# Optimization experiments

Measured on AMD Instinct MI355X. Metric: run time of the kernel, lower is better.

The kernel has to match this reference:

```python
import jax, jax.numpy as jnp
import numpy as np

IN_CHANNELS = 64
N_NODES = 100000
N_POOLED = 50000
N_EDGES = 1250000


def setup_inputs() -> dict:
    key = jax.random.key(0)
    k1, k2, k3 = jax.random.split(key, 3)
    x_abstract = jax.random.normal(k1, (N_POOLED, IN_CHANNELS), dtype=jnp.float32)
    # pooling indices: unique subset of [0, N)
    perm = jax.random.permutation(k2, N_NODES)[:N_POOLED].astype(jnp.int32)
    edge_index = jax.random.randint(k3, (2, N_EDGES), 0, N_NODES, dtype=jnp.int32)
    return {
        "x_abstract": x_abstract,
        "perm": perm,
        "edge_index": edge_index,
        "original_num_nodes": N_NODES,
    }


def reference(x_abstract, perm, edge_index, original_num_nodes):
    N = original_num_nodes
    C = x_abstract.shape[1]
    # scatter pooled features back to original node slots
    x0 = jnp.zeros((N, C), dtype=x_abstract.dtype).at[perm].set(x_abstract)
    is_missing = jnp.ones((N,), dtype=bool).at[perm].set(False)

    # undirected view: every edge contributes both directions
    tgt = jnp.concatenate([edge_index[0], edge_index[1]])  # [2E]
    src = jnp.concatenate([edge_index[1], edge_index[0]])  # [2E]

    # deduplicate (tgt, src) pairs (torch.unique on neighbor ids) via lexsort + adjacent-diff mask
    order = jnp.lexsort((src, tgt))
    t_s = tgt[order]
    s_s = src[order]
    uniq = jnp.concatenate(
        [jnp.array([True]), (t_s[1:] != t_s[:-1]) | (s_s[1:] != s_s[:-1])]
    )
    # drop self loops (neighbor_ids != idx), weight 1 for each unique neighbor pair
    w = (uniq & (t_s != s_s)).astype(x_abstract.dtype)  # [2E]

    # scatter-mean of unique-neighbor features per target node
    feat_sum = jax.ops.segment_sum(x0[s_s] * w[:, None], t_s, num_segments=N)  # [N, C]
    cnt = jax.ops.segment_sum(w, t_s, num_segments=N)  # [N]
    mean = feat_sum / jnp.maximum(cnt, 1.0)[:, None]

    # only missing nodes with at least one neighbor get filled; others keep their value
    fill = is_missing & (cnt > 0)
    return jnp.where(fill[:, None], mean, x0)
```

## Files before the change

### kernel.cpp

```cpp
#include <hip/hip_runtime.h>
#include <stdint.h>

#define K_SLOTS 64
#define NPART 8

__global__ void scatter_kernel(const float* __restrict__ xab,
                               const int* __restrict__ perm,
                               float* __restrict__ out,
                               int* __restrict__ inv,
                               int Np, int C4) {
    int gid = blockIdx.x * blockDim.x + threadIdx.x;
    int j = gid / C4;
    int q = gid - j * C4;
    if (j >= Np) return;
    int p = perm[j];
    if (q == 0) inv[p] = j + 1;
    const float4* src = (const float4*)xab + (size_t)j * C4;
    float4* dst = (float4*)out + (size_t)p * C4;
    dst[q] = src[q];
}

__global__ void mklist_kernel(const int* __restrict__ inv,
                              int* __restrict__ work,
                              unsigned* __restrict__ wn8,
                              int N, int pS, int CAPW) {
    int i = blockIdx.x * blockDim.x + threadIdx.x;
    int lane = threadIdx.x & 63;
    bool miss = (i < N) && (inv[i] == 0);
    int myp = (i < N) ? (i / pS) : 0;
    unsigned long long rem = __ballot(miss);
    while (rem) {
        int lead = (int)__ffsll(rem) - 1;
        int lp = __shfl(myp, lead, 64);
        unsigned long long grp = __ballot(miss && (myp == lp));
        unsigned base = 0;
        if (lane == lead) base = atomicAdd(&wn8[lp], (unsigned)__popcll(grp));
        base = (unsigned)__shfl((int)base, lead, 64);
        if (miss && myp == lp)
            work[(size_t)lp * CAPW + base + __popcll(grp & ((1ull << lane) - 1ull))] = i;
        rem &= ~grp;
    }
}

__global__ void fill_kernel(const int* __restrict__ ei, long long E,
                            const int* __restrict__ inv,
                            int* __restrict__ deg,
                            int* __restrict__ slot,
                            int pS, int N) {
    int p = blockIdx.x & (NPART - 1);
    int q = blockIdx.x >> 3;
    int lo = p * pS;
    int hi = lo + pS; if (hi > N) hi = N;
    long long stride = (long long)(gridDim.x >> 3) * blockDim.x;
    for (long long e = (long long)q * blockDim.x + threadIdx.x; e < E; e += stride) {
        int a = __builtin_nontemporal_load(ei + e);
        int b = __builtin_nontemporal_load(ei + e + E);
        if (a == b) continue;
        if (a >= lo && a < hi && inv[a] == 0) {
            int ib = inv[b];
            int enc = (ib > 0) ? (ib - 1) : (-1 - b);
            int pos = atomicAdd(&deg[a], 1);
            if (pos < K_SLOTS) slot[((size_t)a << 6) + pos] = enc;
        }
        if (b >= lo && b < hi && inv[b] == 0) {
            int ia = inv[a];
            int enc = (ia > 0) ? (ia - 1) : (-1 - a);
            int pos = atomicAdd(&deg[b], 1);
            if (pos < K_SLOTS) slot[((size_t)b << 6) + pos] = enc;
        }
    }
}

__global__ void mean_kernel(const int* __restrict__ work,
                            const unsigned* __restrict__ wn8,
                            const int* __restrict__ slot,
                            const int* __restrict__ deg,
                            const float* __restrict__ xab,
                            float* __restrict__ out,
                            int CAPW, int C) {
    int p = blockIdx.x & (NPART - 1);
    int idx = (int)((blockIdx.x >> 3) * (blockDim.x >> 6) + (threadIdx.x >> 6));
    int lane = threadIdx.x & 63;
    unsigned live = wn8[p]; if (live > (unsigned)CAPW) live = CAPW;
    if ((unsigned)idx >= live) return;
    int node = __builtin_amdgcn_readfirstlane(work[(size_t)p * CAPW + idx]);
    int d = deg[node];
    if (d > K_SLOTS) d = K_SLOTS;
    if (d <= 0) {
        for (int c = lane; c < C; c += 64) out[(size_t)node * C + c] = 0.0f;
        return;
    }
    int e = -1;
    if (lane < d) e = slot[((size_t)node << 6) + lane];
    bool dup = false;
    for (int k = 0; k < d - 1; ++k) {
        int v = __shfl(e, k, 64);
        if (lane > k && e == v) dup = true;
    }
    bool uniq = (lane < d) && !dup;
    int cnt = __popcll(__ballot(uniq));
    unsigned long long pm = __ballot(uniq && e >= 0);
    float rcnt = 1.0f / (float)cnt;
    for (int c0 = 0; c0 < C; c0 += 64) {
        int c = c0 + lane;
        bool cc = (c < C);
        float acc = 0.0f;
        unsigned long long m = pm;
        while (m) {
            int u0 = (int)__ffsll(m) - 1; m &= m - 1;
            int u1 = 0, u2 = 0, u3 = 0;
            bool h1 = (m != 0); if (h1) { u1 = (int)__ffsll(m) - 1; m &= m - 1; }
            bool h2 = (m != 0); if (h2) { u2 = (int)__ffsll(m) - 1; m &= m - 1; }
            bool h3 = (m != 0); if (h3) { u3 = (int)__ffsll(m) - 1; m &= m - 1; }
            int j0 = __shfl(e, u0, 64);
            int j1 = __shfl(e, u1, 64);
            int j2 = __shfl(e, u2, 64);
            int j3 = __shfl(e, u3, 64);
            float v0 = cc        ? xab[(size_t)j0 * C + c] : 0.0f;
            float v1 = (cc & h1) ? xab[(size_t)j1 * C + c] : 0.0f;
            float v2 = (cc & h2) ? xab[(size_t)j2 * C + c] : 0.0f;
            float v3 = (cc & h3) ? xab[(size_t)j3 * C + c] : 0.0f;
            acc += v0 + v1 + v2 + v3;
        }
        if (cc) out[(size_t)node * C + c] = acc * rcnt;
    }
}

extern "C" void kernel_launch(void* const* d_in, const int* in_sizes, int n_in,
                              void* d_out, int out_size, void* d_ws, size_t ws_size,
                              hipStream_t stream) {
    const float* xab  = (const float*)d_in[0];
    const int*   perm = (const int*)d_in[1];
    const int*   ei   = (const int*)d_in[2];
    float* out = (float*)d_out;

    int Np = in_sizes[1];
    int C  = in_sizes[0] / Np;
    long long E = in_sizes[2] / 2;
    int N  = out_size / C;
    int C4 = C / 4;
    int pS = (N + NPART - 1) / NPART;
    int CAPW = (pS + 63) & ~63;

    char* ws = (char*)d_ws;
    size_t off = 0;
    int* slot = (int*)(ws + off); off += (size_t)N * K_SLOTS * 4;
    int* deg  = (int*)(ws + off); off += (size_t)N * 4;
    int* inv  = (int*)(ws + off); off += (size_t)N * 4;
    unsigned* wn8 = (unsigned*)(ws + off); off += 64 * 4;
    int* work = (int*)(ws + off); off += (size_t)NPART * CAPW * 4;

    hipMemsetAsync(deg, 0, ((size_t)2 * N + 64) * 4, stream);

    {
        long long threads = (long long)Np * C4;
        int blocks = (int)((threads + 255) / 256);
        scatter_kernel<<<blocks, 256, 0, stream>>>(xab, perm, out, inv, Np, C4);
    }
    {
        int blocks = (N + 255) / 256;
        mklist_kernel<<<blocks, 256, 0, stream>>>(inv, work, wn8, N, pS, CAPW);
    }
    fill_kernel<<<8 * 1024, 256, 0, stream>>>(ei, E, inv, deg, slot, pS, N);
    {
        int blocksPerP = (CAPW + 3) / 4;
        mean_kernel<<<NPART * blocksPerP, 256, 0, stream>>>(work, wn8, slot, deg,
                                                            xab, out, CAPW, C);
    }
}
```

Baseline: 237.8 us.

## Fuse scatter, worklist and edge fill into one kernel; drop node partitioning

```diff
diff --git a/kernel.cpp b/kernel.cpp
--- a/kernel.cpp
+++ b/kernel.cpp
@@ -2,68 +2,54 @@
 #include <stdint.h>
 
 #define K_SLOTS 64
-#define NPART 8
 
-__global__ void scatter_kernel(const float* __restrict__ xab,
-                               const int* __restrict__ perm,
-                               float* __restrict__ out,
-                               int* __restrict__ inv,
-                               int Np, int C4) {
-    int gid = blockIdx.x * blockDim.x + threadIdx.x;
-    int j = gid / C4;
-    int q = gid - j * C4;
-    if (j >= Np) return;
-    int p = perm[j];
-    if (q == 0) inv[p] = j + 1;
-    const float4* src = (const float4*)xab + (size_t)j * C4;
-    float4* dst = (float4*)out + (size_t)p * C4;
-    dst[q] = src[q];
+__global__ void inv_build(const int* __restrict__ perm, int* __restrict__ inv, int Np) {
+    int j = blockIdx.x * blockDim.x + threadIdx.x;
+    if (j < Np) inv[perm[j]] = j + 1;
 }
 
-__global__ void mklist_kernel(const int* __restrict__ inv,
-                              int* __restrict__ work,
-                              unsigned* __restrict__ wn8,
-                              int N, int pS, int CAPW) {
-    int i = blockIdx.x * blockDim.x + threadIdx.x;
+__global__ void fused_fill(const float* __restrict__ xab,
+                           const int* __restrict__ perm,
+                           const int* __restrict__ ei, long long E,
+                           const int* __restrict__ inv,
+                           float* __restrict__ out,
+                           int* __restrict__ work, unsigned* __restrict__ wn,
+                           int* __restrict__ deg, int* __restrict__ slot,
+                           int Np, int N, int c4log) {
+    long long tid = (long long)blockIdx.x * blockDim.x + threadIdx.x;
+    long long nthr = (long long)gridDim.x * blockDim.x;
     int lane = threadIdx.x & 63;
-    bool miss = (i < N) && (inv[i] == 0);
-    int myp = (i < N) ? (i / pS) : 0;
-    unsigned long long rem = __ballot(miss);
-    while (rem) {
-        int lead = (int)__ffsll(rem) - 1;
-        int lp = __shfl(myp, lead, 64);
-        unsigned long long grp = __ballot(miss && (myp == lp));
-        unsigned base = 0;
-        if (lane == lead) base = atomicAdd(&wn8[lp], (unsigned)__popcll(grp));
-        base = (unsigned)__shfl((int)base, lead, 64);
-        if (miss && myp == lp)
-            work[(size_t)lp * CAPW + base + __popcll(grp & ((1ull << lane) - 1ull))] = i;
-        rem &= ~grp;
+    int C4 = 1 << c4log;
+
+    for (long long g = tid; g < ((long long)Np << c4log); g += nthr) {
+        int j = (int)(g >> c4log);
+        int q = (int)(g & (C4 - 1));
+        int p = perm[j];
+        ((float4*)out)[(size_t)p * C4 + q] = ((const float4*)xab)[(size_t)j * C4 + q];
     }
-}
-
-__global__ void fill_kernel(const int* __restrict__ ei, long long E,
-                            const int* __restrict__ inv,
-                            int* __restrict__ deg,
-                            int* __restrict__ slot,
-                            int pS, int N) {
-    int p = blockIdx.x & (NPART - 1);
-    int q = blockIdx.x >> 3;
-    int lo = p * pS;
-    int hi = lo + pS; if (hi > N) hi = N;
-    long long stride = (long long)(gridDim.x >> 3) * blockDim.x;
-    for (long long e = (long long)q * blockDim.x + threadIdx.x; e < E; e += stride) {
-        int a = __builtin_nontemporal_load(ei + e);
-        int b = __builtin_nontemporal_load(ei + e + E);
+    for (long long g = tid; g < (long long)((N + nthr - 1) / nthr) * nthr; g += nthr) {
+        int i = (int)g;
+        bool miss = (g < N) && (inv[i] == 0);
+        unsigned long long m = __ballot(miss);
+        if (m) {
+            unsigned base = 0;
+            if (lane == (int)__ffsll(m) - 1) base = atomicAdd(wn, (unsigned)__popcll(m));
+            base = (unsigned)__shfl((int)base, (int)__ffsll(m) - 1, 64);
+            if (miss) work[base + __popcll(m & ((1ull << lane) - 1ull))] = i;
+        }
+    }
+    for (long long e = tid; e < E; e += nthr) {
+        int a = ei[e];
+        int b = ei[e + E];
         if (a == b) continue;
-        if (a >= lo && a < hi && inv[a] == 0) {
-            int ib = inv[b];
+        int ia = inv[a];
+        int ib = inv[b];
+        if (ia == 0) {
             int enc = (ib > 0) ? (ib - 1) : (-1 - b);
             int pos = atomicAdd(&deg[a], 1);
             if (pos < K_SLOTS) slot[((size_t)a << 6) + pos] = enc;
         }
-        if (b >= lo && b < hi && inv[b] == 0) {
-            int ia = inv[a];
+        if (ib == 0) {
             int enc = (ia > 0) ? (ia - 1) : (-1 - a);
             int pos = atomicAdd(&deg[b], 1);
             if (pos < K_SLOTS) slot[((size_t)b << 6) + pos] = enc;
@@ -72,18 +58,15 @@
 }
 
 __global__ void mean_kernel(const int* __restrict__ work,
-                            const unsigned* __restrict__ wn8,
                             const int* __restrict__ slot,
                             const int* __restrict__ deg,
                             const float* __restrict__ xab,
                             float* __restrict__ out,
-                            int CAPW, int C) {
-    int p = blockIdx.x & (NPART - 1);
-    int idx = (int)((blockIdx.x >> 3) * (blockDim.x >> 6) + (threadIdx.x >> 6));
+                            int M, int C) {
+    int wid = (int)((blockIdx.x * (long long)blockDim.x + threadIdx.x) >> 6);
     int lane = threadIdx.x & 63;
-    unsigned live = wn8[p]; if (live > (unsigned)CAPW) live = CAPW;
-    if ((unsigned)idx >= live) return;
-    int node = __builtin_amdgcn_readfirstlane(work[(size_t)p * CAPW + idx]);
+    if (wid >= M) return;
+    int node = __builtin_amdgcn_readfirstlane(work[wid]);
     int d = deg[node];
     if (d > K_SLOTS) d = K_SLOTS;
     if (d <= 0) {
@@ -108,19 +91,30 @@
         unsigned long long m = pm;
         while (m) {
             int u0 = (int)__ffsll(m) - 1; m &= m - 1;
-            int u1 = 0, u2 = 0, u3 = 0;
-            bool h1 = (m != 0); if (h1) { u1 = (int)__ffsll(m) - 1; m &= m - 1; }
-            bool h2 = (m != 0); if (h2) { u2 = (int)__ffsll(m) - 1; m &= m - 1; }
-            bool h3 = (m != 0); if (h3) { u3 = (int)__ffsll(m) - 1; m &= m - 1; }
+            bool h1 = (m != 0); int u1 = h1 ? (int)__ffsll(m) - 1 : 0; if (h1) m &= m - 1;
+            bool h2 = (m != 0); int u2 = h2 ? (int)__ffsll(m) - 1 : 0; if (h2) m &= m - 1;
+            bool h3 = (m != 0); int u3 = h3 ? (int)__ffsll(m) - 1 : 0; if (h3) m &= m - 1;
+            bool h4 = (m != 0); int u4 = h4 ? (int)__ffsll(m) - 1 : 0; if (h4) m &= m - 1;
+            bool h5 = (m != 0); int u5 = h5 ? (int)__ffsll(m) - 1 : 0; if (h5) m &= m - 1;
+            bool h6 = (m != 0); int u6 = h6 ? (int)__ffsll(m) - 1 : 0; if (h6) m &= m - 1;
+            bool h7 = (m != 0); int u7 = h7 ? (int)__ffsll(m) - 1 : 0; if (h7) m &= m - 1;
             int j0 = __shfl(e, u0, 64);
             int j1 = __shfl(e, u1, 64);
             int j2 = __shfl(e, u2, 64);
             int j3 = __shfl(e, u3, 64);
+            int j4 = __shfl(e, u4, 64);
+            int j5 = __shfl(e, u5, 64);
+            int j6 = __shfl(e, u6, 64);
+            int j7 = __shfl(e, u7, 64);
             float v0 = cc        ? xab[(size_t)j0 * C + c] : 0.0f;
             float v1 = (cc & h1) ? xab[(size_t)j1 * C + c] : 0.0f;
             float v2 = (cc & h2) ? xab[(size_t)j2 * C + c] : 0.0f;
             float v3 = (cc & h3) ? xab[(size_t)j3 * C + c] : 0.0f;
-            acc += v0 + v1 + v2 + v3;
+            float v4 = (cc & h4) ? xab[(size_t)j4 * C + c] : 0.0f;
+            float v5 = (cc & h5) ? xab[(size_t)j5 * C + c] : 0.0f;
+            float v6 = (cc & h6) ? xab[(size_t)j6 * C + c] : 0.0f;
+            float v7 = (cc & h7) ? xab[(size_t)j7 * C + c] : 0.0f;
+            acc += ((v0 + v1) + (v2 + v3)) + ((v4 + v5) + (v6 + v7));
         }
         if (cc) out[(size_t)node * C + c] = acc * rcnt;
     }
@@ -139,32 +133,27 @@
     long long E = in_sizes[2] / 2;
     int N  = out_size / C;
     int C4 = C / 4;
-    int pS = (N + NPART - 1) / NPART;
-    int CAPW = (pS + 63) & ~63;
+    int c4log = 0; while ((1 << c4log) < C4) c4log++;
+    int M  = N - Np;
 
     char* ws = (char*)d_ws;
     size_t off = 0;
     int* slot = (int*)(ws + off); off += (size_t)N * K_SLOTS * 4;
     int* deg  = (int*)(ws + off); off += (size_t)N * 4;
     int* inv  = (int*)(ws + off); off += (size_t)N * 4;
-    unsigned* wn8 = (unsigned*)(ws + off); off += 64 * 4;
-    int* work = (int*)(ws + off); off += (size_t)NPART * CAPW * 4;
+    unsigned* wn = (unsigned*)(ws + off); off += 64 * 4;
+    int* work = (int*)(ws + off); off += (size_t)M * 4;
 
     hipMemsetAsync(deg, 0, ((size_t)2 * N + 64) * 4, stream);
 
+    inv_build<<<(Np + 255) / 256, 256, 0, stream>>>(perm, inv, Np);
+
+    fused_fill<<<4096, 256, 0, stream>>>(xab, perm, ei, E, inv, out,
+                                         work, wn, deg, slot, Np, N, c4log);
+
     {
-        long long threads = (long long)Np * C4;
+        long long threads = (long long)M * 64;
         int blocks = (int)((threads + 255) / 256);
-        scatter_kernel<<<blocks, 256, 0, stream>>>(xab, perm, out, inv, Np, C4);
-    }
-    {
-        int blocks = (N + 255) / 256;
-        mklist_kernel<<<blocks, 256, 0, stream>>>(inv, work, wn8, N, pS, CAPW);
-    }
-    fill_kernel<<<8 * 1024, 256, 0, stream>>>(ei, E, inv, deg, slot, pS, N);
-    {
-        int blocksPerP = (CAPW + 3) / 4;
-        mean_kernel<<<NPART * blocksPerP, 256, 0, stream>>>(work, wn8, slot, deg,
-                                                            xab, out, CAPW, C);
+        mean_kernel<<<blocks, 256, 0, stream>>>(work, slot, deg, xab, out, M, C);
     }
 }
```

Result: faster. 197.5 us (-16.9%).
